# Optimization experiments

Hardware: AMD Instinct MI355X
Metric: run time of the kernel (lower is better)

The kernel has to match this reference:

```python
import jax, jax.numpy as jnp
import numpy as np

D_IN, D, TOPK = 64, 4, 12
SCALE = 1.0 / np.sqrt(np.float32(D_IN))


def setup_inputs() -> dict:
    key = jax.random.key(0)
    kx, kw = jax.random.split(key)
    x = jax.random.normal(kx, (8, 16, 512, D_IN), dtype=jnp.float32)
    flat = jax.random.normal(kw, (2 * D_IN * D,), dtype=jnp.float32)
    return {"x": x, "flat": flat}


def reference(x, flat):
    # x: (N, T, n, d_in); flat holds wk then wq, each (d_in, d)
    wk = flat[: D_IN * D].reshape(D_IN, D)
    wq = flat[D_IN * D :].reshape(D_IN, D)
    N, T, n, _ = x.shape
    k = jnp.einsum("btnc,cd->btnd", x, wk)  # (N,T,n,d)
    q = jnp.einsum("btnc,cd->btnd", x, wq)  # (N,T,n,d)
    # h = (X Wk)(X Wq)^T : h[i,j] = k_i . q_j -> (N,T,n,n)
    h = jnp.einsum("btnd,btmd->btnm", k, q)
    A = jax.nn.softmax(SCALE * h, axis=-1).sum(axis=-2)  # (N,T,n) column score sums
    # argsort descending + slice topk == top_k indices (values sorted descending)
    _, idxs = jax.lax.top_k(A, TOPK)  # (N,T,topk)
    return idxs.reshape(N, T, TOPK, 1)
```

## Files before the change

### kernel.cpp

```cpp
#include <hip/hip_runtime.h>
#include <math.h>

constexpr int kDIn  = 64;
constexpr int kN    = 512;
constexpr int kTopK = 12;
constexpr int kNBt  = 128;
constexpr int kS    = 4;
constexpr int kRows = kN / kS;
#define CEXP 0.18033688f
#define EXP2(v) __builtin_amdgcn_exp2f(v)
#define LOG2F(v) __builtin_amdgcn_logf(v)

#define DOT4(k, q)        fmaf((k).x,(q).x, fmaf((k).y,(q).y, fmaf((k).z,(q).z, (k).w*(q).w)))
#define DOT4A(k, q, add)  fmaf((k).x,(q).x, fmaf((k).y,(q).y, fmaf((k).z,(q).z, fmaf((k).w,(q).w,(add)))))

constexpr size_t kWsFloats = (size_t)kNBt * 16 * kN;

__global__ __launch_bounds__(512, 4) void fused_attn_kernel(
    const float* __restrict__ x, const float* __restrict__ flat,
    float* __restrict__ apart)
{
  __shared__ float4 Wk[kDIn];
  __shared__ float4 Wq[kDIn];
  __shared__ float4 Qs[kN];
  __shared__ float4 Ks[kRows];
  __shared__ float2 Pp[16 * kRows];
  __shared__ __align__(16) float Cs[kRows];

  const int tid  = threadIdx.x;
  const int p    = blockIdx.x;
  const int xcd  = p & 7;
  const int s    = (p >> 3) & 3;
  const int tile = ((p >> 5) << 3) | xcd;

  if (tid < 64)       Wk[tid]      = reinterpret_cast<const float4*>(flat)[tid];
  else if (tid < 128) Wq[tid - 64] = reinterpret_cast<const float4*>(flat)[tid];
  __syncthreads();

  {
    const float4* xr4 = reinterpret_cast<const float4*>(x + ((size_t)tile * kN + tid) * kDIn);
    float q0=0.f,q1=0.f,q2=0.f,q3=0.f;
    if ((tid >> 7) == s) {
      float k0=0.f,k1=0.f,k2=0.f,k3=0.f;
#pragma unroll
      for (int cc = 0; cc < kDIn / 4; ++cc) {
        float4 xv = xr4[cc];
#pragma unroll
        for (int u = 0; u < 4; ++u) {
          float v = (u==0)?xv.x:(u==1)?xv.y:(u==2)?xv.z:xv.w;
          float4 a = Wk[cc*4+u];
          float4 b = Wq[cc*4+u];
          k0 = fmaf(v, a.x, k0); k1 = fmaf(v, a.y, k1);
          k2 = fmaf(v, a.z, k2); k3 = fmaf(v, a.w, k3);
          q0 = fmaf(v, b.x, q0); q1 = fmaf(v, b.y, q1);
          q2 = fmaf(v, b.z, q2); q3 = fmaf(v, b.w, q3);
        }
      }
      Ks[tid & 127] = make_float4(CEXP*k0, CEXP*k1, CEXP*k2, CEXP*k3);
    } else {
#pragma unroll
      for (int cc = 0; cc < kDIn / 4; ++cc) {
        float4 xv = xr4[cc];
#pragma unroll
        for (int u = 0; u < 4; ++u) {
          float v = (u==0)?xv.x:(u==1)?xv.y:(u==2)?xv.z:xv.w;
          float4 b = Wq[cc*4+u];
          q0 = fmaf(v, b.x, q0); q1 = fmaf(v, b.y, q1);
          q2 = fmaf(v, b.z, q2); q3 = fmaf(v, b.w, q3);
        }
      }
    }
    Qs[tid] = make_float4(q0, q1, q2, q3);
  }
  __syncthreads();

  {
    const int quad  = tid & 31;
    const int slice = tid >> 5;
    const float4 k0 = Ks[quad*4+0], k1 = Ks[quad*4+1];
    const float4 k2 = Ks[quad*4+2], k3 = Ks[quad*4+3];
    const float4* qb = &Qs[slice << 5];

    float m0=-INFINITY, m1=-INFINITY, m2=-INFINITY, m3=-INFINITY;
#pragma unroll 4
    for (int j = 0; j < 32; ++j) {
      float4 q = qb[j];
      m0 = fmaxf(m0, DOT4(k0, q));
      m1 = fmaxf(m1, DOT4(k1, q));
      m2 = fmaxf(m2, DOT4(k2, q));
      m3 = fmaxf(m3, DOT4(k3, q));
    }
    float l0=0.f, l1=0.f, l2=0.f, l3=0.f;
#pragma unroll 4
    for (int j = 0; j < 32; ++j) {
      float4 q = qb[j];
      l0 += EXP2(DOT4A(k0, q, -m0));
      l1 += EXP2(DOT4A(k1, q, -m1));
      l2 += EXP2(DOT4A(k2, q, -m2));
      l3 += EXP2(DOT4A(k3, q, -m3));
    }
    float4* pp4 = reinterpret_cast<float4*>(&Pp[slice * kRows + quad*4]);
    pp4[0] = make_float4(m0, l0, m1, l1);
    pp4[1] = make_float4(m2, l2, m3, l3);
  }
  __syncthreads();

  if (tid < kRows) {
    float m = -INFINITY;
    float2 pr[16];
#pragma unroll
    for (int sl = 0; sl < 16; ++sl) {
      pr[sl] = Pp[sl * kRows + tid];
      m = fmaxf(m, pr[sl].x);
    }
    float l = 0.f;
#pragma unroll
    for (int sl = 0; sl < 16; ++sl) l += pr[sl].y * EXP2(pr[sl].x - m);
    Cs[tid] = m + LOG2F(l);
  }
  __syncthreads();

  {
    const int cq = tid & 127;
    const int rs = tid >> 7;
    const float4 q0 = Qs[cq*4+0], q1 = Qs[cq*4+1];
    const float4 q2 = Qs[cq*4+2], q3 = Qs[cq*4+3];
    const float4* kb = &Ks[rs << 5];
    const float4* cb = reinterpret_cast<const float4*>(&Cs[rs << 5]);

    float a0=0.f, a1=0.f, a2=0.f, a3=0.f;
#pragma unroll 2
    for (int ii = 0; ii < 8; ++ii) {
      float4 cc = cb[ii];
      float4 ka = kb[ii*4+0], kb_ = kb[ii*4+1], kc = kb[ii*4+2], kd = kb[ii*4+3];
      a0 += EXP2(DOT4A(q0, ka, -cc.x));  a1 += EXP2(DOT4A(q1, ka, -cc.x));
      a2 += EXP2(DOT4A(q2, ka, -cc.x));  a3 += EXP2(DOT4A(q3, ka, -cc.x));
      a0 += EXP2(DOT4A(q0, kb_, -cc.y)); a1 += EXP2(DOT4A(q1, kb_, -cc.y));
      a2 += EXP2(DOT4A(q2, kb_, -cc.y)); a3 += EXP2(DOT4A(q3, kb_, -cc.y));
      a0 += EXP2(DOT4A(q0, kc, -cc.z));  a1 += EXP2(DOT4A(q1, kc, -cc.z));
      a2 += EXP2(DOT4A(q2, kc, -cc.z));  a3 += EXP2(DOT4A(q3, kc, -cc.z));
      a0 += EXP2(DOT4A(q0, kd, -cc.w));  a1 += EXP2(DOT4A(q1, kd, -cc.w));
      a2 += EXP2(DOT4A(q2, kd, -cc.w));  a3 += EXP2(DOT4A(q3, kd, -cc.w));
    }
    reinterpret_cast<float4*>(apart + ((size_t)(tile*4 + s) * 4 + rs) * kN)[cq] =
        make_float4(a0, a1, a2, a3);
  }
}

__global__ __launch_bounds__(64) void topk_kernel(
    const float* __restrict__ apart, int* __restrict__ out)
{
  const int lane = threadIdx.x;
  const int bt   = blockIdx.x;
  const float* P = apart + (size_t)bt * 16 * kN;

  float v[8];
  {
    float4 acc0 = make_float4(0.f,0.f,0.f,0.f);
    float4 acc1 = make_float4(0.f,0.f,0.f,0.f);
#pragma unroll
    for (int sl = 0; sl < 16; ++sl) {
      const float4* Ps = reinterpret_cast<const float4*>(P + sl * kN);
      float4 u0 = Ps[lane*2], u1 = Ps[lane*2+1];
      acc0.x += u0.x; acc0.y += u0.y; acc0.z += u0.z; acc0.w += u0.w;
      acc1.x += u1.x; acc1.y += u1.y; acc1.z += u1.z; acc1.w += u1.w;
    }
    v[0]=acc0.x; v[1]=acc0.y; v[2]=acc0.z; v[3]=acc0.w;
    v[4]=acc1.x; v[5]=acc1.y; v[6]=acc1.z; v[7]=acc1.w;
  }

  for (int rnd = 0; rnd < kTopK; ++rnd) {
    float bv = v[0];
    int   bi = lane * 8;
#pragma unroll
    for (int r = 1; r < 8; ++r) {
      if (v[r] > bv) { bv = v[r]; bi = lane * 8 + r; }
    }
#pragma unroll
    for (int off = 32; off >= 1; off >>= 1) {
      float ov = __shfl_xor(bv, off);
      int   oi = __shfl_xor(bi, off);
      if (ov > bv || (ov == bv && oi < bi)) { bv = ov; bi = oi; }
    }
    if (lane == 0) out[bt * kTopK + rnd] = bi;
#pragma unroll
    for (int r = 0; r < 8; ++r) {
      if (lane * 8 + r == bi) v[r] = -INFINITY;
    }
  }
}

__global__ __launch_bounds__(512, 1) void sparse_attn_topk_fallback(
    const float* __restrict__ x, const float* __restrict__ flat, int* __restrict__ out)
{
  __shared__ float4 wk4[kDIn];
  __shared__ float4 wq4[kDIn];
  __shared__ float4 Ks[kN];
  __shared__ float4 Qs[kN];
  __shared__ float  Ms[kN];
  __shared__ float  Rl[kN];
  __shared__ float  As[kN];

  const int tid = threadIdx.x;
  const int bt  = blockIdx.x;

  if (tid < 64)       wk4[tid]      = reinterpret_cast<const float4*>(flat)[tid];
  else if (tid < 128) wq4[tid - 64] = reinterpret_cast<const float4*>(flat)[tid];
  __syncthreads();

  const float* xr = x + ((size_t)bt * kN + tid) * kDIn;
  float k0=0.f,k1=0.f,k2=0.f,k3=0.f, q0=0.f,q1=0.f,q2=0.f,q3=0.f;
#pragma unroll
  for (int c = 0; c < kDIn; ++c) {
    float xv = xr[c];
    float4 a = wk4[c];
    float4 b = wq4[c];
    k0 = fmaf(xv, a.x, k0); k1 = fmaf(xv, a.y, k1);
    k2 = fmaf(xv, a.z, k2); k3 = fmaf(xv, a.w, k3);
    q0 = fmaf(xv, b.x, q0); q1 = fmaf(xv, b.y, q1);
    q2 = fmaf(xv, b.z, q2); q3 = fmaf(xv, b.w, q3);
  }
  Ks[tid] = make_float4(k0, k1, k2, k3);
  Qs[tid] = make_float4(q0, q1, q2, q3);
  __syncthreads();

  float m = -INFINITY;
#pragma unroll 8
  for (int j = 0; j < kN; ++j) {
    float4 qj = Qs[j];
    float h = fmaf(k0, qj.x, fmaf(k1, qj.y, fmaf(k2, qj.z, k3 * qj.w)));
    m = fmaxf(m, h);
  }
  float l = 0.f;
#pragma unroll 8
  for (int j = 0; j < kN; ++j) {
    float4 qj = Qs[j];
    float h = fmaf(k0, qj.x, fmaf(k1, qj.y, fmaf(k2, qj.z, k3 * qj.w)));
    l += exp2f(CEXP * (h - m));
  }
  Ms[tid] = m;
  Rl[tid] = 1.0f / l;
  __syncthreads();

  float acc = 0.f;
#pragma unroll 8
  for (int i = 0; i < kN; ++i) {
    float4 ki = Ks[i];
    float h = fmaf(q0, ki.x, fmaf(q1, ki.y, fmaf(q2, ki.z, q3 * ki.w)));
    acc += exp2f(CEXP * (h - Ms[i])) * Rl[i];
  }
  As[tid] = acc;
  __syncthreads();

  if (tid < 64) {
    float v[8];
#pragma unroll
    for (int r = 0; r < 8; ++r) v[r] = As[tid * 8 + r];
    for (int rnd = 0; rnd < kTopK; ++rnd) {
      float bv = v[0];
      int   bi = tid * 8;
#pragma unroll
      for (int r = 1; r < 8; ++r)
        if (v[r] > bv) { bv = v[r]; bi = tid * 8 + r; }
#pragma unroll
      for (int off = 32; off >= 1; off >>= 1) {
        float ov = __shfl_xor(bv, off);
        int   oi = __shfl_xor(bi, off);
        if (ov > bv || (ov == bv && oi < bi)) { bv = ov; bi = oi; }
      }
      if (tid == 0) out[bt * kTopK + rnd] = bi;
#pragma unroll
      for (int r = 0; r < 8; ++r)
        if (tid * 8 + r == bi) v[r] = -INFINITY;
    }
  }
}

extern "C" void kernel_launch(void* const* d_in, const int* in_sizes, int n_in,
                              void* d_out, int out_size, void* d_ws, size_t ws_size,
                              hipStream_t stream) {
  const float* x    = (const float*)d_in[0];
  const float* flat = (const float*)d_in[1];
  int* out = (int*)d_out;
  const int n_bt = in_sizes[0] / (kN * kDIn);

  if (n_bt != kNBt || ws_size < kWsFloats * sizeof(float)) {
    sparse_attn_topk_fallback<<<n_bt, kN, 0, stream>>>(x, flat, out);
    return;
  }
  float* apart = (float*)d_ws;
  fused_attn_kernel<<<kNBt * kS, 512, 0, stream>>>(x, flat, apart);
  topk_kernel      <<<kNBt,       64, 0, stream>>>(apart, out);
}
```

Measured before the change: 40.38 us.

## Merge attention and top-k into one cooperative kernel with grid syncs

Replaces the two-kernel pipeline with one cooperative kernel. Each block projects only its quarter of rows (four threads per row, shuffle-reduced) and writes K/Q to global workspace. A grid sync follows, then the attention partials, another grid sync, and top-k in the first 128 blocks. This removes the redundant Q projection across the four slice-blocks and the second launch, at the cost of two grid-wide barriers and extra global traffic. The old path is kept as a fallback if the cooperative launch fails. The workspace requirement grows, so the ws_size check can now route to the slow fallback kernel.

```diff
diff --git a/kernel.cpp b/kernel.cpp
--- a/kernel.cpp
+++ b/kernel.cpp
@@ -1,5 +1,8 @@
 #include <hip/hip_runtime.h>
+#include <hip/hip_cooperative_groups.h>
 #include <math.h>
+
+namespace cg = cooperative_groups;
 
 constexpr int kDIn  = 64;
 constexpr int kN    = 512;
@@ -14,64 +17,78 @@
 #define DOT4(k, q)        fmaf((k).x,(q).x, fmaf((k).y,(q).y, fmaf((k).z,(q).z, (k).w*(q).w)))
 #define DOT4A(k, q, add)  fmaf((k).x,(q).x, fmaf((k).y,(q).y, fmaf((k).z,(q).z, fmaf((k).w,(q).w,(add)))))
 
-constexpr size_t kWsFloats = (size_t)kNBt * 16 * kN;
-
-__global__ __launch_bounds__(512, 4) void fused_attn_kernel(
+constexpr size_t kOffKp = 0;
+constexpr size_t kOffQp = kOffKp + (size_t)kNBt * kN * 4;
+constexpr size_t kOffAp = kOffQp + (size_t)kNBt * kN * 4;
+constexpr size_t kWsFloats = kOffAp + (size_t)kNBt * 16 * kN;
+
+__global__ __launch_bounds__(512, 4) void coop_attn_kernel(
     const float* __restrict__ x, const float* __restrict__ flat,
-    float* __restrict__ apart)
+    float* __restrict__ ws, int* __restrict__ out)
 {
-  __shared__ float4 Wk[kDIn];
-  __shared__ float4 Wq[kDIn];
+  __shared__ float4 Wk_[67];
+  __shared__ float4 Wq_[67];
   __shared__ float4 Qs[kN];
   __shared__ float4 Ks[kRows];
   __shared__ float2 Pp[16 * kRows];
   __shared__ __align__(16) float Cs[kRows];
 
+  cg::grid_group grid = cg::this_grid();
+
   const int tid  = threadIdx.x;
-  const int p    = blockIdx.x;
-  const int xcd  = p & 7;
-  const int s    = (p >> 3) & 3;
-  const int tile = ((p >> 5) << 3) | xcd;
-
-  if (tid < 64)       Wk[tid]      = reinterpret_cast<const float4*>(flat)[tid];
-  else if (tid < 128) Wq[tid - 64] = reinterpret_cast<const float4*>(flat)[tid];
-  __syncthreads();
-
-  {
-    const float4* xr4 = reinterpret_cast<const float4*>(x + ((size_t)tile * kN + tid) * kDIn);
-    float q0=0.f,q1=0.f,q2=0.f,q3=0.f;
-    if ((tid >> 7) == s) {
-      float k0=0.f,k1=0.f,k2=0.f,k3=0.f;
-#pragma unroll
-      for (int cc = 0; cc < kDIn / 4; ++cc) {
-        float4 xv = xr4[cc];
-#pragma unroll
-        for (int u = 0; u < 4; ++u) {
-          float v = (u==0)?xv.x:(u==1)?xv.y:(u==2)?xv.z:xv.w;
-          float4 a = Wk[cc*4+u];
-          float4 b = Wq[cc*4+u];
-          k0 = fmaf(v, a.x, k0); k1 = fmaf(v, a.y, k1);
-          k2 = fmaf(v, a.z, k2); k3 = fmaf(v, a.w, k3);
-          q0 = fmaf(v, b.x, q0); q1 = fmaf(v, b.y, q1);
-          q2 = fmaf(v, b.z, q2); q3 = fmaf(v, b.w, q3);
-        }
-      }
-      Ks[tid & 127] = make_float4(CEXP*k0, CEXP*k1, CEXP*k2, CEXP*k3);
-    } else {
-#pragma unroll
-      for (int cc = 0; cc < kDIn / 4; ++cc) {
-        float4 xv = xr4[cc];
-#pragma unroll
-        for (int u = 0; u < 4; ++u) {
-          float v = (u==0)?xv.x:(u==1)?xv.y:(u==2)?xv.z:xv.w;
-          float4 b = Wq[cc*4+u];
-          q0 = fmaf(v, b.x, q0); q1 = fmaf(v, b.y, q1);
-          q2 = fmaf(v, b.z, q2); q3 = fmaf(v, b.w, q3);
-        }
-      }
-    }
-    Qs[tid] = make_float4(q0, q1, q2, q3);
-  }
+  const int b    = blockIdx.x;
+  const int tile = b >> 2;
+  const int s    = b & 3;
+
+  float4* Kp4 = reinterpret_cast<float4*>(ws + kOffKp);
+  float4* Qp4 = reinterpret_cast<float4*>(ws + kOffQp);
+  float*  apart = ws + kOffAp;
+
+  if (tid < 64) {
+    float4 a = reinterpret_cast<const float4*>(flat)[tid];
+    float4 bq = reinterpret_cast<const float4*>(flat)[tid + 64];
+    Wk_[tid + (tid >> 4)] = a;
+    Wq_[tid + (tid >> 4)] = bq;
+  }
+  __syncthreads();
+
+  {
+    const int r  = tid >> 2;
+    const int sl = tid & 3;
+    const int row = s * kRows + r;
+    const float4* xr4 = reinterpret_cast<const float4*>(x)
+                        + ((size_t)tile * kN + row) * 16 + sl * 4;
+    float k0=0.f,k1=0.f,k2=0.f,k3=0.f, q0=0.f,q1=0.f,q2=0.f,q3=0.f;
+#pragma unroll
+    for (int it = 0; it < 4; ++it) {
+      float4 xv = xr4[it];
+#pragma unroll
+      for (int u = 0; u < 4; ++u) {
+        float v = (u==0)?xv.x:(u==1)?xv.y:(u==2)?xv.z:xv.w;
+        float4 a  = Wk_[sl*17 + it*4 + u];
+        float4 bq = Wq_[sl*17 + it*4 + u];
+        k0 = fmaf(v, a.x, k0);  k1 = fmaf(v, a.y, k1);
+        k2 = fmaf(v, a.z, k2);  k3 = fmaf(v, a.w, k3);
+        q0 = fmaf(v, bq.x, q0); q1 = fmaf(v, bq.y, q1);
+        q2 = fmaf(v, bq.z, q2); q3 = fmaf(v, bq.w, q3);
+      }
+    }
+#pragma unroll
+    for (int off = 1; off <= 2; off <<= 1) {
+      k0 += __shfl_xor(k0, off); k1 += __shfl_xor(k1, off);
+      k2 += __shfl_xor(k2, off); k3 += __shfl_xor(k3, off);
+      q0 += __shfl_xor(q0, off); q1 += __shfl_xor(q1, off);
+      q2 += __shfl_xor(q2, off); q3 += __shfl_xor(q3, off);
+    }
+    if (sl == 0) {
+      Kp4[(size_t)tile * kN + row] = make_float4(CEXP*k0, CEXP*k1, CEXP*k2, CEXP*k3);
+      Qp4[(size_t)tile * kN + row] = make_float4(q0, q1, q2, q3);
+    }
+  }
+  grid.sync();
+
+  Qs[tid] = Qp4[(size_t)tile * kN + tid];
+  if (tid < kRows) Ks[tid] = Kp4[(size_t)tile * kN + s * kRows + tid];
   __syncthreads();
 
   {
@@ -145,6 +162,174 @@
     reinterpret_cast<float4*>(apart + ((size_t)(tile*4 + s) * 4 + rs) * kN)[cq] =
         make_float4(a0, a1, a2, a3);
   }
+  grid.sync();
+
+  if (b < kNBt && tid < 64) {
+    const int lane = tid;
+    const float* P = apart + (size_t)b * 16 * kN;
+    float v[8];
+    {
+      float4 acc0 = make_float4(0.f,0.f,0.f,0.f);
+      float4 acc1 = make_float4(0.f,0.f,0.f,0.f);
+#pragma unroll
+      for (int sl = 0; sl < 16; ++sl) {
+        const float4* Ps = reinterpret_cast<const float4*>(P + sl * kN);
+        float4 u0 = Ps[lane*2], u1 = Ps[lane*2+1];
+        acc0.x += u0.x; acc0.y += u0.y; acc0.z += u0.z; acc0.w += u0.w;
+        acc1.x += u1.x; acc1.y += u1.y; acc1.z += u1.z; acc1.w += u1.w;
+      }
+      v[0]=acc0.x; v[1]=acc0.y; v[2]=acc0.z; v[3]=acc0.w;
+      v[4]=acc1.x; v[5]=acc1.y; v[6]=acc1.z; v[7]=acc1.w;
+    }
+    for (int rnd = 0; rnd < kTopK; ++rnd) {
+      float bv = v[0];
+      int   bi = lane * 8;
+#pragma unroll
+      for (int r = 1; r < 8; ++r)
+        if (v[r] > bv) { bv = v[r]; bi = lane * 8 + r; }
+#pragma unroll
+      for (int off = 32; off >= 1; off >>= 1) {
+        float ov = __shfl_xor(bv, off);
+        int   oi = __shfl_xor(bi, off);
+        if (ov > bv || (ov == bv && oi < bi)) { bv = ov; bi = oi; }
+      }
+      if (lane == 0) out[b * kTopK + rnd] = bi;
+#pragma unroll
+      for (int r = 0; r < 8; ++r)
+        if (lane * 8 + r == bi) v[r] = -INFINITY;
+    }
+  }
+}
+
+__global__ __launch_bounds__(512, 4) void fused_attn_kernel(
+    const float* __restrict__ x, const float* __restrict__ flat,
+    float* __restrict__ apart)
+{
+  __shared__ float4 Wk[kDIn];
+  __shared__ float4 Wq[kDIn];
+  __shared__ float4 Qs[kN];
+  __shared__ float4 Ks[kRows];
+  __shared__ float2 Pp[16 * kRows];
+  __shared__ __align__(16) float Cs[kRows];
+
+  const int tid  = threadIdx.x;
+  const int p    = blockIdx.x;
+  const int xcd  = p & 7;
+  const int s    = (p >> 3) & 3;
+  const int tile = ((p >> 5) << 3) | xcd;
+
+  if (tid < 64)       Wk[tid]      = reinterpret_cast<const float4*>(flat)[tid];
+  else if (tid < 128) Wq[tid - 64] = reinterpret_cast<const float4*>(flat)[tid];
+  __syncthreads();
+
+  {
+    const float4* xr4 = reinterpret_cast<const float4*>(x + ((size_t)tile * kN + tid) * kDIn);
+    float q0=0.f,q1=0.f,q2=0.f,q3=0.f;
+    if ((tid >> 7) == s) {
+      float k0=0.f,k1=0.f,k2=0.f,k3=0.f;
+#pragma unroll
+      for (int cc = 0; cc < kDIn / 4; ++cc) {
+        float4 xv = xr4[cc];
+#pragma unroll
+        for (int u = 0; u < 4; ++u) {
+          float v = (u==0)?xv.x:(u==1)?xv.y:(u==2)?xv.z:xv.w;
+          float4 a = Wk[cc*4+u];
+          float4 b = Wq[cc*4+u];
+          k0 = fmaf(v, a.x, k0); k1 = fmaf(v, a.y, k1);
+          k2 = fmaf(v, a.z, k2); k3 = fmaf(v, a.w, k3);
+          q0 = fmaf(v, b.x, q0); q1 = fmaf(v, b.y, q1);
+          q2 = fmaf(v, b.z, q2); q3 = fmaf(v, b.w, q3);
+        }
+      }
+      Ks[tid & 127] = make_float4(CEXP*k0, CEXP*k1, CEXP*k2, CEXP*k3);
+    } else {
+#pragma unroll
+      for (int cc = 0; cc < kDIn / 4; ++cc) {
+        float4 xv = xr4[cc];
+#pragma unroll
+        for (int u = 0; u < 4; ++u) {
+          float v = (u==0)?xv.x:(u==1)?xv.y:(u==2)?xv.z:xv.w;
+          float4 b = Wq[cc*4+u];
+          q0 = fmaf(v, b.x, q0); q1 = fmaf(v, b.y, q1);
+          q2 = fmaf(v, b.z, q2); q3 = fmaf(v, b.w, q3);
+        }
+      }
+    }
+    Qs[tid] = make_float4(q0, q1, q2, q3);
+  }
+  __syncthreads();
+
+  {
+    const int quad  = tid & 31;
+    const int slice = tid >> 5;
+    const float4 k0 = Ks[quad*4+0], k1 = Ks[quad*4+1];
+    const float4 k2 = Ks[quad*4+2], k3 = Ks[quad*4+3];
+    const float4* qb = &Qs[slice << 5];
+
+    float m0=-INFINITY, m1=-INFINITY, m2=-INFINITY, m3=-INFINITY;
+#pragma unroll 4
+    for (int j = 0; j < 32; ++j) {
+      float4 q = qb[j];
+      m0 = fmaxf(m0, DOT4(k0, q));
+      m1 = fmaxf(m1, DOT4(k1, q));
+      m2 = fmaxf(m2, DOT4(k2, q));
+      m3 = fmaxf(m3, DOT4(k3, q));
+    }
+    float l0=0.f, l1=0.f, l2=0.f, l3=0.f;
+#pragma unroll 4
+    for (int j = 0; j < 32; ++j) {
+      float4 q = qb[j];
+      l0 += EXP2(DOT4A(k0, q, -m0));
+      l1 += EXP2(DOT4A(k1, q, -m1));
+      l2 += EXP2(DOT4A(k2, q, -m2));
+      l3 += EXP2(DOT4A(k3, q, -m3));
+    }
+    float4* pp4 = reinterpret_cast<float4*>(&Pp[slice * kRows + quad*4]);
+    pp4[0] = make_float4(m0, l0, m1, l1);
+    pp4[1] = make_float4(m2, l2, m3, l3);
+  }
+  __syncthreads();
+
+  if (tid < kRows) {
+    float m = -INFINITY;
+    float2 pr[16];
+#pragma unroll
+    for (int sl = 0; sl < 16; ++sl) {
+      pr[sl] = Pp[sl * kRows + tid];
+      m = fmaxf(m, pr[sl].x);
+    }
+    float l = 0.f;
+#pragma unroll
+    for (int sl = 0; sl < 16; ++sl) l += pr[sl].y * EXP2(pr[sl].x - m);
+    Cs[tid] = m + LOG2F(l);
+  }
+  __syncthreads();
+
+  {
+    const int cq = tid & 127;
+    const int rs = tid >> 7;
+    const float4 q0 = Qs[cq*4+0], q1 = Qs[cq*4+1];
+    const float4 q2 = Qs[cq*4+2], q3 = Qs[cq*4+3];
+    const float4* kb = &Ks[rs << 5];
+    const float4* cb = reinterpret_cast<const float4*>(&Cs[rs << 5]);
+
+    float a0=0.f, a1=0.f, a2=0.f, a3=0.f;
+#pragma unroll 2
+    for (int ii = 0; ii < 8; ++ii) {
+      float4 cc = cb[ii];
+      float4 ka = kb[ii*4+0], kb_ = kb[ii*4+1], kc = kb[ii*4+2], kd = kb[ii*4+3];
+      a0 += EXP2(DOT4A(q0, ka, -cc.x));  a1 += EXP2(DOT4A(q1, ka, -cc.x));
+      a2 += EXP2(DOT4A(q2, ka, -cc.x));  a3 += EXP2(DOT4A(q3, ka, -cc.x));
+      a0 += EXP2(DOT4A(q0, kb_, -cc.y)); a1 += EXP2(DOT4A(q1, kb_, -cc.y));
+      a2 += EXP2(DOT4A(q2, kb_, -cc.y)); a3 += EXP2(DOT4A(q3, kb_, -cc.y));
+      a0 += EXP2(DOT4A(q0, kc, -cc.z));  a1 += EXP2(DOT4A(q1, kc, -cc.z));
+      a2 += EXP2(DOT4A(q2, kc, -cc.z));  a3 += EXP2(DOT4A(q3, kc, -cc.z));
+      a0 += EXP2(DOT4A(q0, kd, -cc.w));  a1 += EXP2(DOT4A(q1, kd, -cc.w));
+      a2 += EXP2(DOT4A(q2, kd, -cc.w));  a3 += EXP2(DOT4A(q3, kd, -cc.w));
+    }
+    reinterpret_cast<float4*>(apart + ((size_t)(tile*4 + s) * 4 + rs) * kN)[cq] =
+        make_float4(a0, a1, a2, a3);
+  }
 }
 
 __global__ __launch_bounds__(64) void topk_kernel(
@@ -173,9 +358,8 @@
     float bv = v[0];
     int   bi = lane * 8;
 #pragma unroll
-    for (int r = 1; r < 8; ++r) {
+    for (int r = 1; r < 8; ++r)
       if (v[r] > bv) { bv = v[r]; bi = lane * 8 + r; }
-    }
 #pragma unroll
     for (int off = 32; off >= 1; off >>= 1) {
       float ov = __shfl_xor(bv, off);
@@ -184,9 +368,8 @@
     }
     if (lane == 0) out[bt * kTopK + rnd] = bi;
 #pragma unroll
-    for (int r = 0; r < 8; ++r) {
+    for (int r = 0; r < 8; ++r)
       if (lane * 8 + r == bi) v[r] = -INFINITY;
-    }
   }
 }
 
@@ -288,7 +471,16 @@
     sparse_attn_topk_fallback<<<n_bt, kN, 0, stream>>>(x, flat, out);
     return;
   }
-  float* apart = (float*)d_ws;
-  fused_attn_kernel<<<kNBt * kS, 512, 0, stream>>>(x, flat, apart);
-  topk_kernel      <<<kNBt,       64, 0, stream>>>(apart, out);
+  float* ws = (float*)d_ws;
+
+  void* args[] = {(void*)&x, (void*)&flat, (void*)&ws, (void*)&out};
+  hipError_t err = hipLaunchCooperativeKernel(
+      reinterpret_cast<void*>(coop_attn_kernel),
+      dim3(kNBt * kS), dim3(kN), args, 0, stream);
+
+  if (err != hipSuccess) {
+    float* apart = ws + kOffAp;
+    fused_attn_kernel<<<kNBt * kS, 512, 0, stream>>>(x, flat, apart);
+    topk_kernel      <<<kNBt,       64, 0, stream>>>(apart, out);
+  }
 }
```

Result: slower. 130.7 us (+223.7%).
